# Kernel optimization log

Hardware: AMD Instinct MI355X
Metric: run time of the kernel (lower is better)

Reference implementation:

```python
import jax, jax.numpy as jnp
import numpy as np

N_USERS, N_BOOKS, D, E, B = 50000, 100000, 128, 500000, 16384
N = N_USERS + N_BOOKS
EPS = 1e-5


def _gcn_conv(x, W, b, src, dst, n):
    # PyG GCNConv: linear transform, then symmetric-normalized aggregation with self-loops.
    h = x @ W  # [N, D]
    ones = jnp.ones(src.shape[0], h.dtype)
    deg = jax.ops.segment_sum(ones, dst, num_segments=n) + 1.0  # +1 for self-loop
    dis = jax.lax.rsqrt(deg)  # deg^{-1/2}
    norm = dis[src] * dis[dst]  # [E]
    agg = jax.ops.segment_sum(h[src] * norm[:, None], dst, num_segments=n)
    agg = agg + h * (dis * dis)[:, None]  # self-loop contribution, norm = deg_i^{-1}
    return agg + b


def _batch_norm(x, gamma, beta):
    m = x.mean(axis=0)
    v = x.var(axis=0)  # biased, as in torch BN normalization
    return (x - m) * jax.lax.rsqrt(v + EPS) * gamma + beta


def setup_inputs() -> dict:
    key = jax.random.key(0)
    ks = jax.random.split(key, 12)
    edge_index = jax.random.randint(ks[0], (2, E), 0, N)
    x = jax.random.normal(ks[1], (1, 1), dtype=jnp.float32)  # unused by forward
    src_nodes = jax.random.randint(ks[2], (B,), 0, N_USERS)
    dst_nodes = jax.random.randint(ks[3], (B,), N_USERS, N)
    user_emb = 0.01 * jax.random.normal(ks[4], (N_USERS, D), dtype=jnp.float32)
    book_emb = 0.01 * jax.random.normal(ks[5], (N_BOOKS, D), dtype=jnp.float32)
    s = 1.0 / np.sqrt(D)
    W1 = jax.random.uniform(ks[6], (D, D), jnp.float32, -s, s)
    b1 = jnp.zeros((D,), jnp.float32)
    W2 = jax.random.uniform(ks[7], (D, D), jnp.float32, -s, s)
    b2 = jnp.zeros((D,), jnp.float32)
    g1 = jnp.ones((D,), jnp.float32)
    be1 = jnp.zeros((D,), jnp.float32)
    g2 = jnp.ones((D,), jnp.float32)
    be2 = jnp.zeros((D,), jnp.float32)
    return {"edge_index": edge_index, "x": x, "src_nodes": src_nodes,
            "dst_nodes": dst_nodes, "user_emb": user_emb, "book_emb": book_emb,
            "W1": W1, "b1": b1, "g1": g1, "be1": be1,
            "W2": W2, "b2": b2, "g2": g2, "be2": be2}


def reference(edge_index, x, src_nodes, dst_nodes, user_emb, book_emb,
              W1, b1, g1, be1, W2, b2, g2, be2):
    esrc, edst = edge_index[0], edge_index[1]
    h = jnp.concatenate([user_emb, book_emb], axis=0)  # [N, D]
    h = _gcn_conv(h, W1, b1, esrc, edst, N)
    h = jax.nn.relu(_batch_norm(h, g1, be1))
    h = _gcn_conv(h, W2, b2, esrc, edst, N)
    h = jax.nn.relu(_batch_norm(h, g2, be2))
    ratings = jnp.sum(h[src_nodes] * h[dst_nodes], axis=1)  # [B]
    return ratings
```

## Files before the change

### kernel.cpp

```cpp
#include <hip/hip_runtime.h>
#include <hip/hip_bf16.h>

#define NN      150000
#define NUSERS  50000
#define DD      128
#define EE      500000
#define BB      16384
#define NSLICE  32
#define ESTRIDE 32

using short8  = __attribute__((ext_vector_type(8))) short;
using ushort8 = __attribute__((ext_vector_type(8))) unsigned short;
using f32x4   = __attribute__((ext_vector_type(4))) float;

typedef __attribute__((address_space(1))) const unsigned int glb_u32;
typedef __attribute__((address_space(3))) unsigned int       lds_u32;

__device__ __forceinline__ short f2bf(float v) {
    __hip_bfloat16 b = __float2bfloat16(v);
    return __builtin_bit_cast(short, b);
}
__device__ __forceinline__ float bf2f(unsigned short b) {
    return __uint_as_float(((unsigned)b) << 16);
}

__global__ __launch_bounds__(256) void prep_k(int4* __restrict__ zbase, int zn4, int zb,
                                              const float* __restrict__ W1,
                                              const float* __restrict__ W2,
                                              short* __restrict__ F1,
                                              short* __restrict__ F2) {
    int b = blockIdx.x;
    if (b < zb) {
        int i = b * 256 + threadIdx.x;
        if (i < zn4) zbase[i] = make_int4(0, 0, 0, 0);
        return;
    }
    int idx = (b - zb) * 256 + threadIdx.x;
    int m = idx >> 14;
    int i = idx & 16383;
    int e  = i & 7;
    int l  = (i >> 3) & 63;
    int kk = (i >> 9) & 3;
    int ct = i >> 11;
    int k = kk * 32 + (l >> 4) * 8 + e;
    int c = ct * 16 + (l & 15);
    const float* W = m ? W2 : W1;
    short*       F = m ? F2 : F1;
    F[i] = f2bf(W[k * DD + c]);
}

__global__ __launch_bounds__(256) void count_k(const int* __restrict__ dst,
                                               int* __restrict__ cnt,
                                               const int* __restrict__ srcn,
                                               const int* __restrict__ dstn,
                                               unsigned char* __restrict__ flags) {
    int e = blockIdx.x * 256 + threadIdx.x;
    if (e < EE) atomicAdd(&cnt[dst[e]], 1);
    if (e < BB) { flags[srcn[e]] = 1; flags[dstn[e]] = 1; }
}

__global__ __launch_bounds__(256) void fill_k(const int* __restrict__ src,
                                              const int* __restrict__ dst,
                                              const int* __restrict__ cnt,
                                              int* __restrict__ cur,
                                              int2* __restrict__ sedge) {
    int e = blockIdx.x * 256 + threadIdx.x;
    if (e < EE) {
        int d = dst[e], s = src[e];
        int pos = atomicAdd(&cur[d], 1);
        if (pos > ESTRIDE - 1) pos = ESTRIDE - 1;
        float w = rsqrtf((float)cnt[s] + 1.0f);
        sedge[(size_t)d * ESTRIDE + pos] = make_int2(s, __float_as_int(w));
    }
}

template<int MODE>
__global__ __launch_bounds__(128) void gemm_mfma_k(const float* __restrict__ A0,
                                                   const float* __restrict__ A1,
                                                   int nsplit,
                                                   const unsigned short* __restrict__ Ab,
                                                   const float* __restrict__ coefs,
                                                   const short* __restrict__ Wfrag,
                                                   unsigned short* __restrict__ hout) {
    constexpr int ROWB  = (MODE == 0) ? 528 : 272;
    constexpr int PAY   = (MODE == 0) ? 512 : 256;
    constexpr int TILEB = 32 * ROWB;
    constexpr int NCH   = TILEB / 16;
    constexpr int FULLR = NCH / 128;

    __shared__ __align__(16) char smem[TILEB];

    int t    = threadIdx.x;
    int wave = t >> 6;
    int lane = t & 63;
    int kgrp = lane >> 4;
    int lrow = lane & 15;
    int r0   = blockIdx.x * 32;

#pragma unroll
    for (int r = 0; r < FULLR; ++r) {
        int chunk = r * 128 + t;
        int o     = chunk * 16;
        int row   = o / ROWB;
        int inner = o - row * ROWB;
        if (inner >= PAY) inner = 0;
        int gr = r0 + row; if (gr > NN - 1) gr = NN - 1;
        const char* src;
        if (MODE == 0) src = (const char*)((gr < nsplit) ? (A0 + (size_t)gr * DD)
                                                         : (A1 + (size_t)(gr - nsplit) * DD)) + inner;
        else           src = (const char*)(Ab + (size_t)gr * DD) + inner;
        lds_u32* dst = (lds_u32*)(smem + (r * 128 + wave * 64) * 16);
        __builtin_amdgcn_global_load_lds((glb_u32*)src, dst, 16, 0, 0);
    }
    if (wave == 0 && lane < 32) {
        int chunk = FULLR * 128 + lane;
        int o     = chunk * 16;
        int row   = o / ROWB;
        int inner = o - row * ROWB;
        if (inner >= PAY) inner = 0;
        int gr = r0 + row; if (gr > NN - 1) gr = NN - 1;
        const char* src;
        if (MODE == 0) src = (const char*)((gr < nsplit) ? (A0 + (size_t)gr * DD)
                                                         : (A1 + (size_t)(gr - nsplit) * DD)) + inner;
        else           src = (const char*)(Ab + (size_t)gr * DD) + inner;
        lds_u32* dst = (lds_u32*)(smem + FULLR * 128 * 16);
        __builtin_amdgcn_global_load_lds((glb_u32*)src, dst, 16, 0, 0);
    }
    __syncthreads();

    const char* arow = smem + (wave * 16 + lrow) * ROWB;

    f32x4 acc[8];
#pragma unroll
    for (int ct = 0; ct < 8; ++ct) acc[ct] = (f32x4){0.f, 0.f, 0.f, 0.f};

    const short8* wf = (const short8*)Wfrag;

#pragma unroll
    for (int kk = 0; kk < 4; ++kk) {
        short8 rfrag;
        if (MODE == 0) {
            f32x4 va = *(const f32x4*)(arow + kk * 128 + kgrp * 32);
            f32x4 vb = *(const f32x4*)(arow + kk * 128 + kgrp * 32 + 16);
#pragma unroll
            for (int j = 0; j < 4; ++j) { rfrag[j] = f2bf(va[j]); rfrag[4 + j] = f2bf(vb[j]); }
        } else {
            int d0 = kk * 32 + kgrp * 8;
            ushort8 u = *(const ushort8*)(arow + kk * 64 + kgrp * 16);
            f32x4 s1 = *(const f32x4*)(coefs + d0);
            f32x4 s2 = *(const f32x4*)(coefs + d0 + 4);
            f32x4 t1 = *(const f32x4*)(coefs + 128 + d0);
            f32x4 t2 = *(const f32x4*)(coefs + 128 + d0 + 4);
#pragma unroll
            for (int j = 0; j < 4; ++j) {
                rfrag[j]     = f2bf(fmaxf(bf2f(u[j])     * s1[j] + t1[j], 0.f));
                rfrag[4 + j] = f2bf(fmaxf(bf2f(u[4 + j]) * s2[j] + t2[j], 0.f));
            }
        }
#pragma unroll
        for (int ct = 0; ct < 8; ++ct) {
            short8 wfr = wf[(ct * 4 + kk) * 64 + lane];
            acc[ct] = __builtin_amdgcn_mfma_f32_16x16x32_bf16(wfr, rfrag, acc[ct], 0, 0, 0);
        }
    }

    int row = r0 + wave * 16 + lrow;
    if (row < NN) {
        size_t rb = (size_t)row * DD;
#pragma unroll
        for (int ct = 0; ct < 8; ++ct) {
            int col = ct * 16 + kgrp * 4;
            unsigned p0 = (unsigned)(unsigned short)f2bf(acc[ct][0])
                        | ((unsigned)(unsigned short)f2bf(acc[ct][1]) << 16);
            unsigned p1 = (unsigned)(unsigned short)f2bf(acc[ct][2])
                        | ((unsigned)(unsigned short)f2bf(acc[ct][3]) << 16);
            uint2 p; p.x = p0; p.y = p1;
            *(uint2*)(hout + rb + col) = p;
        }
    }
}

template<int PRUNE>
__global__ __launch_bounds__(256) void gather_k(const unsigned short* __restrict__ h,
                                                const int2* __restrict__ sedge,
                                                const int* __restrict__ cnt,
                                                const unsigned char* __restrict__ flags,
                                                unsigned short* __restrict__ aggb,
                                                float* __restrict__ sums) {
    int t = threadIdx.x;
    int l = t & 15;
    int rg = t >> 4;
    int row = blockIdx.x * 16 + rg;
    int len = cnt[row];
    const int2* se = sedge + (size_t)row * ESTRIDE;
    const ushort8* hp = (const ushort8*)h;

    float acc[8];
#pragma unroll
    for (int j = 0; j < 8; ++j) acc[j] = 0.f;

    for (int base = 0; base < len; base += 4) {
        int i1 = min(base + 1, len - 1);
        int i2 = min(base + 2, len - 1);
        int i3 = min(base + 3, len - 1);
        int2 e0 = se[base], e1 = se[i1], e2 = se[i2], e3 = se[i3];
        ushort8 h0 = hp[(size_t)e0.x * 16 + l];
        ushort8 h1 = hp[(size_t)e1.x * 16 + l];
        ushort8 h2 = hp[(size_t)e2.x * 16 + l];
        ushort8 h3 = hp[(size_t)e3.x * 16 + l];
        float w0 = __int_as_float(e0.y);
        float w1 = (base + 1 < len) ? __int_as_float(e1.y) : 0.f;
        float w2 = (base + 2 < len) ? __int_as_float(e2.y) : 0.f;
        float w3 = (base + 3 < len) ? __int_as_float(e3.y) : 0.f;
#pragma unroll
        for (int j = 0; j < 8; ++j) {
            acc[j] += w0 * bf2f(h0[j]) + w1 * bf2f(h1[j])
                    + w2 * bf2f(h2[j]) + w3 * bf2f(h3[j]);
        }
    }
    float d  = rsqrtf((float)len + 1.0f);
    float d2 = d * d;
    ushort8 hs = hp[(size_t)row * 16 + l];
    float r[8];
    ushort8 o;
#pragma unroll
    for (int j = 0; j < 8; ++j) {
        r[j] = d * acc[j] + d2 * bf2f(hs[j]);
        o[j] = (unsigned short)f2bf(r[j]);
    }
    if (!PRUNE || flags[row])
        ((ushort8*)aggb)[(size_t)row * 16 + l] = o;

    __shared__ float red[16][128];
    float* slice = sums + (blockIdx.x & (NSLICE - 1)) * 256;
    int co = l * 8;
#pragma unroll
    for (int j = 0; j < 8; ++j) red[rg][co + j] = r[j];
    __syncthreads();
    if (t < 128) {
        float a = 0.f;
#pragma unroll
        for (int g = 0; g < 16; ++g) a += red[g][t];
        atomicAdd(&slice[t], a);
    }
    __syncthreads();
#pragma unroll
    for (int j = 0; j < 8; ++j) red[rg][co + j] = r[j] * r[j];
    __syncthreads();
    if (t < 128) {
        float a = 0.f;
#pragma unroll
        for (int g = 0; g < 16; ++g) a += red[g][t];
        atomicAdd(&slice[128 + t], a);
    }
}

__global__ void bncoef_k(const float* __restrict__ sums,
                         const float* __restrict__ gamma,
                         const float* __restrict__ beta,
                         float* __restrict__ coefs) {
    int c = threadIdx.x;
    if (c >= DD) return;
    float s = 0.f, s2 = 0.f;
#pragma unroll
    for (int g = 0; g < NSLICE; ++g) {
        s  += sums[g * 256 + c];
        s2 += sums[g * 256 + 128 + c];
    }
    const float n = (float)NN;
    float m  = s / n;
    float v  = s2 / n - m * m;
    float is = rsqrtf(v + 1e-5f);
    float sc = gamma[c] * is;
    coefs[c] = sc;
    coefs[128 + c] = beta[c] - m * sc;
}

__global__ __launch_bounds__(256) void ratings_k(const unsigned short* __restrict__ x,
                                                 const int* __restrict__ srcn,
                                                 const int* __restrict__ dstn,
                                                 const float* __restrict__ coefs,
                                                 float* __restrict__ out) {
    int wid  = (blockIdx.x * 256 + threadIdx.x) >> 6;
    int lane = threadIdx.x & 63;
    if (wid >= BB) return;
    int u = srcn[wid], v = dstn[wid];
    const ushort2* xp = (const ushort2*)x;
    ushort2 a = xp[(size_t)u * 64 + lane];
    ushort2 b = xp[(size_t)v * 64 + lane];
    float2 sc = ((const float2*)coefs)[lane];
    float2 sh = ((const float2*)(coefs + 128))[lane];
    float ax = fmaxf(bf2f(a.x) * sc.x + sh.x, 0.f);
    float ay = fmaxf(bf2f(a.y) * sc.y + sh.y, 0.f);
    float bx = fmaxf(bf2f(b.x) * sc.x + sh.x, 0.f);
    float by = fmaxf(bf2f(b.y) * sc.y + sh.y, 0.f);
    float acc = ax * bx + ay * by;
#pragma unroll
    for (int off = 32; off; off >>= 1) acc += __shfl_down(acc, off, 64);
    if (lane == 0) out[wid] = acc;
}

extern "C" void kernel_launch(void* const* d_in, const int* in_sizes, int n_in,
                              void* d_out, int out_size, void* d_ws, size_t ws_size,
                              hipStream_t stream) {
    const int*   edge  = (const int*)d_in[0];
    const int*   esrc  = edge;
    const int*   edst  = edge + EE;
    const int*   srcn  = (const int*)d_in[2];
    const int*   dstn  = (const int*)d_in[3];
    const float* uemb  = (const float*)d_in[4];
    const float* bemb  = (const float*)d_in[5];
    const float* W1    = (const float*)d_in[6];
    const float* g1    = (const float*)d_in[8];
    const float* be1   = (const float*)d_in[9];
    const float* W2    = (const float*)d_in[10];
    const float* g2    = (const float*)d_in[12];
    const float* be2   = (const float*)d_in[13];
    float* out = (float*)d_out;

    unsigned short* aggb   = (unsigned short*)d_ws;
    unsigned short* hbuf   = aggb + (size_t)NN * DD;
    int*            cnt    = (int*)(hbuf + (size_t)NN * DD);
    int*            cur    = cnt + 150016;
    unsigned char*  flags  = (unsigned char*)(cur + 150016);
    float*          sums1  = (float*)(flags + 150016);
    float*          sums2  = sums1 + NSLICE * 256;
    int2*           sedge  = (int2*)(sums2 + NSLICE * 256);
    short*          Wf1    = (short*)(sedge + (size_t)150016 * ESTRIDE);
    short*          Wf2    = Wf1 + 16384;
    float*          coef1  = (float*)(Wf2 + 16384);
    float*          coef2  = coef1 + 256;

    const int zn4   = (150016 + 150016 + 150016 / 4 + 2 * NSLICE * 256) / 4;
    const int zb    = (zn4 + 255) / 256;
    const int egrid = (EE + 255) / 256;
    const int ggrid = (NN + 31) / 32;
    const int agrid = NN / 16;

    prep_k<<<zb + 128, 256, 0, stream>>>((int4*)cnt, zn4, zb, W1, W2, Wf1, Wf2);
    count_k<<<egrid, 256, 0, stream>>>(edst, cnt, srcn, dstn, flags);
    fill_k<<<egrid, 256, 0, stream>>>(esrc, edst, cnt, cur, sedge);

    gemm_mfma_k<0><<<ggrid, 128, 0, stream>>>(uemb, bemb, NUSERS, nullptr, nullptr, Wf1, hbuf);
    gather_k<0><<<agrid, 256, 0, stream>>>(hbuf, sedge, cnt, flags, aggb, sums1);
    bncoef_k<<<1, 128, 0, stream>>>(sums1, g1, be1, coef1);

    gemm_mfma_k<1><<<ggrid, 128, 0, stream>>>(nullptr, nullptr, 0, aggb, coef1, Wf2, hbuf);
    gather_k<1><<<agrid, 256, 0, stream>>>(hbuf, sedge, cnt, flags, aggb, sums2);
    bncoef_k<<<1, 128, 0, stream>>>(sums2, g2, be2, coef2);

    ratings_k<<<BB / 4, 256, 0, stream>>>(aggb, srcn, dstn, coef2, out);
}
```

Baseline: 192.7 us.

## Merge degree count and edge fill into one pass, compute norms in gather

The separate count and fill kernels become one kernel, in which the atomic slot counter also serves as the in-degree, removing the second counter array and one launch. Bucketed edges now store only the source index (int instead of int2), and the gather kernel computes the per-source normalization from cnt on the fly. This halves edge-bucket traffic and drops a full edge pass, at the cost of extra dependent cnt loads and rsqrt work inside the gather loops, which run twice. Buckets are still capped at ESTRIDE entries, and the self-normalization uses the full degree.

```diff
diff --git a/kernel.cpp b/kernel.cpp
--- a/kernel.cpp
+++ b/kernel.cpp
@@ -49,29 +49,21 @@
     F[i] = f2bf(W[k * DD + c]);
 }
 
-__global__ __launch_bounds__(256) void count_k(const int* __restrict__ dst,
-                                               int* __restrict__ cnt,
-                                               const int* __restrict__ srcn,
-                                               const int* __restrict__ dstn,
-                                               unsigned char* __restrict__ flags) {
-    int e = blockIdx.x * 256 + threadIdx.x;
-    if (e < EE) atomicAdd(&cnt[dst[e]], 1);
-    if (e < BB) { flags[srcn[e]] = 1; flags[dstn[e]] = 1; }
-}
-
-__global__ __launch_bounds__(256) void fill_k(const int* __restrict__ src,
-                                              const int* __restrict__ dst,
-                                              const int* __restrict__ cnt,
-                                              int* __restrict__ cur,
-                                              int2* __restrict__ sedge) {
+__global__ __launch_bounds__(256) void countfill_k(const int* __restrict__ src,
+                                                   const int* __restrict__ dst,
+                                                   int* __restrict__ cnt,
+                                                   int* __restrict__ sedge,
+                                                   const int* __restrict__ srcn,
+                                                   const int* __restrict__ dstn,
+                                                   unsigned char* __restrict__ flags) {
     int e = blockIdx.x * 256 + threadIdx.x;
     if (e < EE) {
         int d = dst[e], s = src[e];
-        int pos = atomicAdd(&cur[d], 1);
+        int pos = atomicAdd(&cnt[d], 1);
         if (pos > ESTRIDE - 1) pos = ESTRIDE - 1;
-        float w = rsqrtf((float)cnt[s] + 1.0f);
-        sedge[(size_t)d * ESTRIDE + pos] = make_int2(s, __float_as_int(w));
-    }
+        sedge[(size_t)d * ESTRIDE + pos] = s;
+    }
+    if (e < BB) { flags[srcn[e]] = 1; flags[dstn[e]] = 1; }
 }
 
 template<int MODE>
@@ -182,7 +174,7 @@
 
 template<int PRUNE>
 __global__ __launch_bounds__(256) void gather_k(const unsigned short* __restrict__ h,
-                                                const int2* __restrict__ sedge,
+                                                const int* __restrict__ sedge,
                                                 const int* __restrict__ cnt,
                                                 const unsigned char* __restrict__ flags,
                                                 unsigned short* __restrict__ aggb,
@@ -191,8 +183,9 @@
     int l = t & 15;
     int rg = t >> 4;
     int row = blockIdx.x * 16 + rg;
-    int len = cnt[row];
-    const int2* se = sedge + (size_t)row * ESTRIDE;
+    int deg = cnt[row];
+    int len = min(deg, ESTRIDE);
+    const int* se = sedge + (size_t)row * ESTRIDE;
     const ushort8* hp = (const ushort8*)h;
 
     float acc[8];
@@ -203,22 +196,22 @@
         int i1 = min(base + 1, len - 1);
         int i2 = min(base + 2, len - 1);
         int i3 = min(base + 3, len - 1);
-        int2 e0 = se[base], e1 = se[i1], e2 = se[i2], e3 = se[i3];
-        ushort8 h0 = hp[(size_t)e0.x * 16 + l];
-        ushort8 h1 = hp[(size_t)e1.x * 16 + l];
-        ushort8 h2 = hp[(size_t)e2.x * 16 + l];
-        ushort8 h3 = hp[(size_t)e3.x * 16 + l];
-        float w0 = __int_as_float(e0.y);
-        float w1 = (base + 1 < len) ? __int_as_float(e1.y) : 0.f;
-        float w2 = (base + 2 < len) ? __int_as_float(e2.y) : 0.f;
-        float w3 = (base + 3 < len) ? __int_as_float(e3.y) : 0.f;
+        int s0 = se[base], s1 = se[i1], s2 = se[i2], s3 = se[i3];
+        ushort8 h0 = hp[(size_t)s0 * 16 + l];
+        ushort8 h1 = hp[(size_t)s1 * 16 + l];
+        ushort8 h2 = hp[(size_t)s2 * 16 + l];
+        ushort8 h3 = hp[(size_t)s3 * 16 + l];
+        float w0 = rsqrtf((float)cnt[s0] + 1.0f);
+        float w1 = (base + 1 < len) ? rsqrtf((float)cnt[s1] + 1.0f) : 0.f;
+        float w2 = (base + 2 < len) ? rsqrtf((float)cnt[s2] + 1.0f) : 0.f;
+        float w3 = (base + 3 < len) ? rsqrtf((float)cnt[s3] + 1.0f) : 0.f;
 #pragma unroll
         for (int j = 0; j < 8; ++j) {
             acc[j] += w0 * bf2f(h0[j]) + w1 * bf2f(h1[j])
                     + w2 * bf2f(h2[j]) + w3 * bf2f(h3[j]);
         }
     }
-    float d  = rsqrtf((float)len + 1.0f);
+    float d  = rsqrtf((float)deg + 1.0f);
     float d2 = d * d;
     ushort8 hs = hp[(size_t)row * 16 + l];
     float r[8];
@@ -321,25 +314,23 @@
     unsigned short* aggb   = (unsigned short*)d_ws;
     unsigned short* hbuf   = aggb + (size_t)NN * DD;
     int*            cnt    = (int*)(hbuf + (size_t)NN * DD);
-    int*            cur    = cnt + 150016;
-    unsigned char*  flags  = (unsigned char*)(cur + 150016);
+    unsigned char*  flags  = (unsigned char*)(cnt + 150016);
     float*          sums1  = (float*)(flags + 150016);
     float*          sums2  = sums1 + NSLICE * 256;
-    int2*           sedge  = (int2*)(sums2 + NSLICE * 256);
+    int*            sedge  = (int*)(sums2 + NSLICE * 256);
     short*          Wf1    = (short*)(sedge + (size_t)150016 * ESTRIDE);
     short*          Wf2    = Wf1 + 16384;
     float*          coef1  = (float*)(Wf2 + 16384);
     float*          coef2  = coef1 + 256;
 
-    const int zn4   = (150016 + 150016 + 150016 / 4 + 2 * NSLICE * 256) / 4;
+    const int zn4   = (150016 * 4 + 150016 + 2 * NSLICE * 256 * 4) / 16;
     const int zb    = (zn4 + 255) / 256;
     const int egrid = (EE + 255) / 256;
     const int ggrid = (NN + 31) / 32;
     const int agrid = NN / 16;
 
     prep_k<<<zb + 128, 256, 0, stream>>>((int4*)cnt, zn4, zb, W1, W2, Wf1, Wf2);
-    count_k<<<egrid, 256, 0, stream>>>(edst, cnt, srcn, dstn, flags);
-    fill_k<<<egrid, 256, 0, stream>>>(esrc, edst, cnt, cur, sedge);
+    countfill_k<<<egrid, 256, 0, stream>>>(esrc, edst, cnt, sedge, srcn, dstn, flags);
 
     gemm_mfma_k<0><<<ggrid, 128, 0, stream>>>(uemb, bemb, NUSERS, nullptr, nullptr, Wf1, hbuf);
     gather_k<0><<<agrid, 256, 0, stream>>>(hbuf, sedge, cnt, flags, aggb, sums1);
```

New measurement: 175.3 us. -9.0%, faster.
